# Kernel tuning notes

Hardware: AMD Instinct MI355X
Metric: run time of the kernel (lower is better)

Reference implementation:

```python
import jax, jax.numpy as jnp
import numpy as np
from jax import lax

B, T, N = 512, 512, 64  # batch, max_seq_len, num_tags


def setup_inputs() -> dict:
    key = jax.random.key(0)
    k1, k2, k3, k4 = jax.random.split(key, 4)
    inputs = jax.random.normal(k1, (B, T, N), dtype=jnp.float32)
    transition_params = jax.random.normal(k2, (N, N), dtype=jnp.float32)
    tag_indices = jax.random.randint(k3, (B, T), 0, N, dtype=jnp.int32)
    sequence_lengths = jax.random.randint(k4, (B,), 0, T, dtype=jnp.int32)
    return {
        "inputs": inputs,
        "transition_params": transition_params,
        "tag_indices": tag_indices,
        "sequence_lengths": sequence_lengths,
    }


def _crf_log_norm(inputs, transition_params, sequence_lengths):
    # inputs: [B, T, N]
    first = inputs[:, 0, :]                       # alpha after first token, [B, N]
    rest = jnp.transpose(inputs[:, 1:, :], (1, 0, 2))  # [T-1, B, N]

    def step(alpha, emit):
        # alpha: [B, N] -> broadcast-add transitions [N, N], logsumexp over prev tag
        new = emit + jax.nn.logsumexp(alpha[:, :, None] + transition_params[None], axis=1)
        return new, new

    _, alphas = lax.scan(step, first, rest)       # [T-1, B, N]
    all_alphas = jnp.concatenate([first[None], alphas], axis=0)  # [T, B, N]
    all_alphas = jnp.transpose(all_alphas, (1, 0, 2))            # [B, T, N]
    last_index = jnp.maximum(0, sequence_lengths - 1)            # [B]
    alpha_last = jnp.take_along_axis(all_alphas, last_index[:, None, None], axis=1)[:, 0, :]
    return jax.nn.logsumexp(alpha_last, axis=1)   # [B]


def _crf_sequence_score(inputs, tag_indices, sequence_lengths, transition_params):
    mask = (jnp.arange(T)[None, :] < sequence_lengths[:, None]).astype(inputs.dtype)  # [B, T]
    # unary: gather emission score of the gold tag at each position
    unary = jnp.take_along_axis(inputs, tag_indices[:, :, None], axis=2)[:, :, 0]      # [B, T]
    unary_scores = jnp.sum(unary * mask, axis=1)
    # binary: transition scores between consecutive gold tags
    binary = transition_params[tag_indices[:, :-1], tag_indices[:, 1:]]                # [B, T-1]
    binary_scores = jnp.sum(binary * mask[:, 1:], axis=1)
    return unary_scores + binary_scores


def reference(inputs, transition_params, tag_indices, sequence_lengths):
    tag_indices = tag_indices.astype(jnp.int32)
    sequence_lengths = sequence_lengths.astype(jnp.int32)
    sequence_scores = _crf_sequence_score(inputs, tag_indices, sequence_lengths, transition_params)
    log_norm = _crf_log_norm(inputs, transition_params, sequence_lengths)
    log_likelihood = sequence_scores - log_norm   # [B]
    return (log_likelihood, transition_params)
```

## Files before the change

### kernel.cpp

```cpp
#include <hip/hip_runtime.h>

#define BB 512
#define TT 512
#define NN 64

__device__ __forceinline__ float readlane_f(float v, int lane) {
    return __int_as_float(__builtin_amdgcn_readlane(__float_as_int(v), lane));
}


#define S2(x) #x
#define S1(x) S2(x)
#define RLX(SR, L) "v_readlane_b32 " SR ", %4, " S1(L) "\n\t"

#define SCLOB "s40","s41","s42","s43","s44","s45","s46","s47", \
              "s48","s49","s50","s51","s52","s53","s54","s55"

#define GRP0() \
    asm volatile( \
        "s_nop 4\n\t" \
        RLX("s40", 0)  RLX("s41", 1)  RLX("s42", 2)  RLX("s43", 3)  \
        RLX("s44", 4)  RLX("s45", 5)  RLX("s46", 6)  RLX("s47", 7)  \
        RLX("s48", 8)  RLX("s49", 9)  RLX("s50", 10) RLX("s51", 11) \
        RLX("s52", 12) RLX("s53", 13) RLX("s54", 14) RLX("s55", 15) \
        "v_pk_mul_f32 %0, s[40:41], %5\n\t" \
        "v_pk_mul_f32 %1, s[42:43], %6\n\t" \
        "v_pk_mul_f32 %2, s[44:45], %7\n\t" \
        "v_pk_mul_f32 %3, s[46:47], %8\n\t" \
        "v_pk_fma_f32 %0, s[48:49], %9,  %0\n\t" \
        "v_pk_fma_f32 %1, s[50:51], %10, %1\n\t" \
        "v_pk_fma_f32 %2, s[52:53], %11, %2\n\t" \
        "v_pk_fma_f32 %3, s[54:55], %12, %3\n\t" \
        : "=&v"(a0), "=&v"(a1), "=&v"(a2), "=&v"(a3) \
        : "v"(q), \
          "v"(EP[0]), "v"(EP[1]), "v"(EP[2]), "v"(EP[3]), \
          "v"(EP[4]), "v"(EP[5]), "v"(EP[6]), "v"(EP[7]) \
        : SCLOB);

#define GRPN(G) \
    asm volatile( \
        RLX("s40", (G)*16+0)  RLX("s41", (G)*16+1)  RLX("s42", (G)*16+2)  RLX("s43", (G)*16+3)  \
        RLX("s44", (G)*16+4)  RLX("s45", (G)*16+5)  RLX("s46", (G)*16+6)  RLX("s47", (G)*16+7)  \
        RLX("s48", (G)*16+8)  RLX("s49", (G)*16+9)  RLX("s50", (G)*16+10) RLX("s51", (G)*16+11) \
        RLX("s52", (G)*16+12) RLX("s53", (G)*16+13) RLX("s54", (G)*16+14) RLX("s55", (G)*16+15) \
        "v_pk_fma_f32 %0, s[40:41], %5,  %0\n\t" \
        "v_pk_fma_f32 %1, s[42:43], %6,  %1\n\t" \
        "v_pk_fma_f32 %2, s[44:45], %7,  %2\n\t" \
        "v_pk_fma_f32 %3, s[46:47], %8,  %3\n\t" \
        "v_pk_fma_f32 %0, s[48:49], %9,  %0\n\t" \
        "v_pk_fma_f32 %1, s[50:51], %10, %1\n\t" \
        "v_pk_fma_f32 %2, s[52:53], %11, %2\n\t" \
        "v_pk_fma_f32 %3, s[54:55], %12, %3\n\t" \
        : "+v"(a0), "+v"(a1), "+v"(a2), "+v"(a3) \
        : "v"(q), \
          "v"(EP[8*(G)+0]), "v"(EP[8*(G)+1]), "v"(EP[8*(G)+2]), "v"(EP[8*(G)+3]), \
          "v"(EP[8*(G)+4]), "v"(EP[8*(G)+5]), "v"(EP[8*(G)+6]), "v"(EP[8*(G)+7]) \
        : SCLOB);

#define STEP(tc_, EM) { \
    float2 a0, a1, a2, a3; \
    GRP0() GRPN(1) GRPN(2) GRPN(3) \
    const float sdot = ((a0.x + a0.y) + (a1.x + a1.y)) \
                     + ((a2.x + a2.y) + (a3.x + a3.y)); \
    const float s0v = readlane_f(sdot, 0); \
    const int   k   = ((__float_as_int(s0v) >> 23) & 255) - 127; \
    const bool  act = (tc_) <= last; \
    kcum += act ? k : 0; \
    const float qn = (EM) * ldexpf(sdot, -k); \
    q = act ? qn : q; \
}

__global__ __launch_bounds__(64, 1) void crf_kernel(
    const float* __restrict__ inputs,
    const float* __restrict__ trans,
    const int*   __restrict__ tags,
    const int*   __restrict__ lens,
    float*       __restrict__ out)
{
    const int b = blockIdx.x;
    const int j = threadIdx.x;

    if (b < 64) out[BB + b * 64 + j] = trans[b * 64 + j];

    const int L    = lens[b];
    const int last = (L - 1) > 0 ? (L - 1) : 0;

    const float* inb  = inputs + (size_t)b * TT * NN;
    const int*   tagb = tags + (size_t)b * TT;

    float sc = 0.f;
    #pragma unroll
    for (int k = 0; k < 8; ++k) {
        const int t  = k * 64 + j;
        const int tg = tagb[t];
        if (t < L) sc += inb[t * NN + tg];
        if (t + 1 < L) sc += trans[tg * NN + tagb[t + 1]];
    }
    #pragma unroll
    for (int x = 32; x >= 1; x >>= 1) sc += __shfl_xor(sc, x, 64);

    float2 EP[32];
    #pragma unroll
    for (int g = 0; g < 32; ++g) {
        EP[g].x = __expf(trans[(2 * g)     * NN + j]);
        EP[g].y = __expf(trans[(2 * g + 1) * NN + j]);
    }

    const float alpha0 = inb[j];
    const float m0 = readlane_f(alpha0, 0);
    float q = __expf(alpha0 - m0);
    int kcum = 0;

    float4 fA0, fA1, fB0, fB1;

#define LD(vec, comp, tt) { const int tc_ = (tt) <= last ? (tt) : last; \
                            vec.comp = inb[tc_ * NN + j]; }
#define LOAD8(v0, v1, base) \
    LD(v0, x, (base) + 0) LD(v0, y, (base) + 1) LD(v0, z, (base) + 2) LD(v0, w, (base) + 3) \
    LD(v1, x, (base) + 4) LD(v1, y, (base) + 5) LD(v1, z, (base) + 6) LD(v1, w, (base) + 7)
#define EXP8(v0, v1) \
    v0.x = __expf(v0.x); v0.y = __expf(v0.y); v0.z = __expf(v0.z); v0.w = __expf(v0.w); \
    v1.x = __expf(v1.x); v1.y = __expf(v1.y); v1.z = __expf(v1.z); v1.w = __expf(v1.w);

    LOAD8(fA0, fA1, 1)
    EXP8(fA0, fA1)

    for (int t0 = 1; t0 <= last; t0 += 16) {
        LOAD8(fB0, fB1, t0 + 8)
        STEP(t0 + 0, fA0.x) STEP(t0 + 1, fA0.y) STEP(t0 + 2, fA0.z) STEP(t0 + 3, fA0.w)
        STEP(t0 + 4, fA1.x) STEP(t0 + 5, fA1.y) STEP(t0 + 6, fA1.z) STEP(t0 + 7, fA1.w)
        EXP8(fB0, fB1)
        LOAD8(fA0, fA1, t0 + 16)
        STEP(t0 + 8,  fB0.x) STEP(t0 + 9,  fB0.y) STEP(t0 + 10, fB0.z) STEP(t0 + 11, fB0.w)
        STEP(t0 + 12, fB1.x) STEP(t0 + 13, fB1.y) STEP(t0 + 14, fB1.z) STEP(t0 + 15, fB1.w)
        EXP8(fA0, fA1)
    }
#undef EXP8
#undef LOAD8
#undef LD

    float qs = q;
    #pragma unroll
    for (int x = 32; x >= 1; x >>= 1) qs += __shfl_xor(qs, x, 64);
    if (j == 0) {
        const double C = (double)m0 + (double)kcum * 0.6931471805599453;
        out[b] = sc - (float)((double)__logf(qs) + C);
    }
}

extern "C" void kernel_launch(void* const* d_in, const int* in_sizes, int n_in,
                              void* d_out, int out_size, void* d_ws, size_t ws_size,
                              hipStream_t stream) {
    const float* inputs = (const float*)d_in[0];
    const float* trans  = (const float*)d_in[1];
    const int*   tags   = (const int*)d_in[2];
    const int*   lens   = (const int*)d_in[3];
    float*       out    = (float*)d_out;

    crf_kernel<<<dim3(BB), dim3(64), 0, stream>>>(inputs, trans, tags, lens, out);
}
```

Baseline: 237.6 us.

## Replace readlane broadcast matvec with DPP row-rotate FMAs and sparse rescaling

The per-timestep 64x64 exp-domain matvec no longer broadcasts q through 64 v_readlane instructions into scalar registers. Instead it uses three ds_bpermute calls to fetch q from the other 16-lane rows and v_fmac_f32_dpp with row_ror to rotate within each row. The exp-transition matrix is preloaded in a permuted layout matching the DPP rotation direction, which is detected at runtime. Power-of-two rescaling now runs every 4th step instead of every step, cutting readlane and exponent work but risking float overflow or underflow between rescales.

```diff
diff --git a/kernel.cpp b/kernel.cpp
--- a/kernel.cpp
+++ b/kernel.cpp
@@ -11,63 +11,57 @@
 
 #define S2(x) #x
 #define S1(x) S2(x)
-#define RLX(SR, L) "v_readlane_b32 " SR ", %4, " S1(L) "\n\t"
 
-#define SCLOB "s40","s41","s42","s43","s44","s45","s46","s47", \
-              "s48","s49","s50","s51","s52","s53","s54","s55"
+#define FMAC_DPP(ACC, QB, EV, R) \
+    asm("v_fmac_f32_dpp %0, %1, %2 row_ror:" S1(R) " row_mask:0xf bank_mask:0xf" \
+        : "+v"(ACC) : "v"(QB), "v"(EV));
+#define MUL_DPP(DST, QB, EV, R) \
+    asm("v_mul_f32_dpp %0, %1, %2 row_ror:" S1(R) " row_mask:0xf bank_mask:0xf" \
+        : "=v"(DST) : "v"(QB), "v"(EV));
 
-#define GRP0() \
-    asm volatile( \
-        "s_nop 4\n\t" \
-        RLX("s40", 0)  RLX("s41", 1)  RLX("s42", 2)  RLX("s43", 3)  \
-        RLX("s44", 4)  RLX("s45", 5)  RLX("s46", 6)  RLX("s47", 7)  \
-        RLX("s48", 8)  RLX("s49", 9)  RLX("s50", 10) RLX("s51", 11) \
-        RLX("s52", 12) RLX("s53", 13) RLX("s54", 14) RLX("s55", 15) \
-        "v_pk_mul_f32 %0, s[40:41], %5\n\t" \
-        "v_pk_mul_f32 %1, s[42:43], %6\n\t" \
-        "v_pk_mul_f32 %2, s[44:45], %7\n\t" \
-        "v_pk_mul_f32 %3, s[46:47], %8\n\t" \
-        "v_pk_fma_f32 %0, s[48:49], %9,  %0\n\t" \
-        "v_pk_fma_f32 %1, s[50:51], %10, %1\n\t" \
-        "v_pk_fma_f32 %2, s[52:53], %11, %2\n\t" \
-        "v_pk_fma_f32 %3, s[54:55], %12, %3\n\t" \
-        : "=&v"(a0), "=&v"(a1), "=&v"(a2), "=&v"(a3) \
-        : "v"(q), \
-          "v"(EP[0]), "v"(EP[1]), "v"(EP[2]), "v"(EP[3]), \
-          "v"(EP[4]), "v"(EP[5]), "v"(EP[6]), "v"(EP[7]) \
-        : SCLOB);
+#define BLK_FIRST(QB, C0, C1, C2, C3) \
+    a0 = QB * C0.x; \
+    MUL_DPP(a1, QB, C0.y, 1)  MUL_DPP(a2, QB, C0.z, 2)  MUL_DPP(a3, QB, C0.w, 3) \
+    FMAC_DPP(a0, QB, C1.x, 4)  FMAC_DPP(a1, QB, C1.y, 5) \
+    FMAC_DPP(a2, QB, C1.z, 6)  FMAC_DPP(a3, QB, C1.w, 7) \
+    FMAC_DPP(a0, QB, C2.x, 8)  FMAC_DPP(a1, QB, C2.y, 9) \
+    FMAC_DPP(a2, QB, C2.z, 10) FMAC_DPP(a3, QB, C2.w, 11) \
+    FMAC_DPP(a0, QB, C3.x, 12) FMAC_DPP(a1, QB, C3.y, 13) \
+    FMAC_DPP(a2, QB, C3.z, 14) FMAC_DPP(a3, QB, C3.w, 15)
 
-#define GRPN(G) \
-    asm volatile( \
-        RLX("s40", (G)*16+0)  RLX("s41", (G)*16+1)  RLX("s42", (G)*16+2)  RLX("s43", (G)*16+3)  \
-        RLX("s44", (G)*16+4)  RLX("s45", (G)*16+5)  RLX("s46", (G)*16+6)  RLX("s47", (G)*16+7)  \
-        RLX("s48", (G)*16+8)  RLX("s49", (G)*16+9)  RLX("s50", (G)*16+10) RLX("s51", (G)*16+11) \
-        RLX("s52", (G)*16+12) RLX("s53", (G)*16+13) RLX("s54", (G)*16+14) RLX("s55", (G)*16+15) \
-        "v_pk_fma_f32 %0, s[40:41], %5,  %0\n\t" \
-        "v_pk_fma_f32 %1, s[42:43], %6,  %1\n\t" \
-        "v_pk_fma_f32 %2, s[44:45], %7,  %2\n\t" \
-        "v_pk_fma_f32 %3, s[46:47], %8,  %3\n\t" \
-        "v_pk_fma_f32 %0, s[48:49], %9,  %0\n\t" \
-        "v_pk_fma_f32 %1, s[50:51], %10, %1\n\t" \
-        "v_pk_fma_f32 %2, s[52:53], %11, %2\n\t" \
-        "v_pk_fma_f32 %3, s[54:55], %12, %3\n\t" \
-        : "+v"(a0), "+v"(a1), "+v"(a2), "+v"(a3) \
-        : "v"(q), \
-          "v"(EP[8*(G)+0]), "v"(EP[8*(G)+1]), "v"(EP[8*(G)+2]), "v"(EP[8*(G)+3]), \
-          "v"(EP[8*(G)+4]), "v"(EP[8*(G)+5]), "v"(EP[8*(G)+6]), "v"(EP[8*(G)+7]) \
-        : SCLOB);
+#define BLK(QB, C0, C1, C2, C3) \
+    a0 = fmaf(QB, C0.x, a0); \
+    FMAC_DPP(a1, QB, C0.y, 1)  FMAC_DPP(a2, QB, C0.z, 2)  FMAC_DPP(a3, QB, C0.w, 3) \
+    FMAC_DPP(a0, QB, C1.x, 4)  FMAC_DPP(a1, QB, C1.y, 5) \
+    FMAC_DPP(a2, QB, C1.z, 6)  FMAC_DPP(a3, QB, C1.w, 7) \
+    FMAC_DPP(a0, QB, C2.x, 8)  FMAC_DPP(a1, QB, C2.y, 9) \
+    FMAC_DPP(a2, QB, C2.z, 10) FMAC_DPP(a3, QB, C2.w, 11) \
+    FMAC_DPP(a0, QB, C3.x, 12) FMAC_DPP(a1, QB, C3.y, 13) \
+    FMAC_DPP(a2, QB, C3.z, 14) FMAC_DPP(a3, QB, C3.w, 15)
 
-#define STEP(tc_, EM) { \
-    float2 a0, a1, a2, a3; \
-    GRP0() GRPN(1) GRPN(2) GRPN(3) \
-    const float sdot = ((a0.x + a0.y) + (a1.x + a1.y)) \
-                     + ((a2.x + a2.y) + (a3.x + a3.y)); \
-    const float s0v = readlane_f(sdot, 0); \
-    const int   k   = ((__float_as_int(s0v) >> 23) & 255) - 127; \
-    const bool  act = (tc_) <= last; \
-    kcum += act ? k : 0; \
-    const float qn = (EM) * ldexpf(sdot, -k); \
-    q = act ? qn : q; \
+#define STEP(tc_, EM, RESC) { \
+    asm("s_nop 1" : "+v"(q));    \
+    const int qi = __float_as_int(q); \
+    const float q1 = __int_as_float(__builtin_amdgcn_ds_bpermute(a16, qi)); \
+    const float q2 = __int_as_float(__builtin_amdgcn_ds_bpermute(a32, qi)); \
+    const float q3 = __int_as_float(__builtin_amdgcn_ds_bpermute(a48, qi)); \
+    float a0, a1, a2, a3; \
+    BLK_FIRST(q, D00, D01, D02, D03) \
+    BLK(q1, D10, D11, D12, D13) \
+    BLK(q2, D20, D21, D22, D23) \
+    BLK(q3, D30, D31, D32, D33) \
+    const float s = (a0 + a1) + (a2 + a3); \
+    float qn; \
+    if (RESC) { \
+        const int sb = __float_as_int(readlane_f(s, 0)); \
+        const int kb = ((sb >> 23) & 255) - 127; \
+        const float sf = __int_as_float((127 - kb) << 23);   \
+        qn = (s * (EM)) * sf; \
+        if ((tc_) <= last) kcum += kb; \
+    } else { \
+        qn = s * (EM); \
+    } \
+    q = ((tc_) <= last) ? qn : q; \
 }
 
 __global__ __launch_bounds__(64, 1) void crf_kernel(
@@ -99,12 +93,29 @@
     #pragma unroll
     for (int x = 32; x >= 1; x >>= 1) sc += __shfl_xor(sc, x, 64);
 
-    float2 EP[32];
-    #pragma unroll
-    for (int g = 0; g < 32; ++g) {
-        EP[g].x = __expf(trans[(2 * g)     * NN + j]);
-        EP[g].y = __expf(trans[(2 * g + 1) * NN + j]);
-    }
+    const int pr  = __builtin_amdgcn_update_dpp(0, j, 0x121 ,
+                                                0xf, 0xf, false);
+    const int r0p = __builtin_amdgcn_readlane(pr, 0);
+    const int dhw = (r0p == 1) ? 1 : -1;
+
+    float4 D00, D01, D02, D03, D10, D11, D12, D13;
+    float4 D20, D21, D22, D23, D30, D31, D32, D33;
+#define LDD(DST, B, R) { \
+    const int rr = (j + dhw * (R)) & 15; \
+    const int ii = (((j & 48) | rr) + 16 * (B)) & 63; \
+    DST = __expf(trans[ii * NN + j]); }
+#define LDD4(V, B, R0) LDD(V.x, B, R0) LDD(V.y, B, (R0)+1) \
+                       LDD(V.z, B, (R0)+2) LDD(V.w, B, (R0)+3)
+    LDD4(D00, 0, 0) LDD4(D01, 0, 4) LDD4(D02, 0, 8) LDD4(D03, 0, 12)
+    LDD4(D10, 1, 0) LDD4(D11, 1, 4) LDD4(D12, 1, 8) LDD4(D13, 1, 12)
+    LDD4(D20, 2, 0) LDD4(D21, 2, 4) LDD4(D22, 2, 8) LDD4(D23, 2, 12)
+    LDD4(D30, 3, 0) LDD4(D31, 3, 4) LDD4(D32, 3, 8) LDD4(D33, 3, 12)
+#undef LDD4
+#undef LDD
+
+    const int a16 = ((j + 16) & 63) * 4;
+    const int a32 = ((j + 32) & 63) * 4;
+    const int a48 = ((j + 48) & 63) * 4;
 
     const float alpha0 = inb[j];
     const float m0 = readlane_f(alpha0, 0);
@@ -127,12 +138,16 @@
 
     for (int t0 = 1; t0 <= last; t0 += 16) {
         LOAD8(fB0, fB1, t0 + 8)
-        STEP(t0 + 0, fA0.x) STEP(t0 + 1, fA0.y) STEP(t0 + 2, fA0.z) STEP(t0 + 3, fA0.w)
-        STEP(t0 + 4, fA1.x) STEP(t0 + 5, fA1.y) STEP(t0 + 6, fA1.z) STEP(t0 + 7, fA1.w)
+        STEP(t0 + 0, fA0.x, 0) STEP(t0 + 1, fA0.y, 0)
+        STEP(t0 + 2, fA0.z, 0) STEP(t0 + 3, fA0.w, 1)
+        STEP(t0 + 4, fA1.x, 0) STEP(t0 + 5, fA1.y, 0)
+        STEP(t0 + 6, fA1.z, 0) STEP(t0 + 7, fA1.w, 1)
         EXP8(fB0, fB1)
         LOAD8(fA0, fA1, t0 + 16)
-        STEP(t0 + 8,  fB0.x) STEP(t0 + 9,  fB0.y) STEP(t0 + 10, fB0.z) STEP(t0 + 11, fB0.w)
-        STEP(t0 + 12, fB1.x) STEP(t0 + 13, fB1.y) STEP(t0 + 14, fB1.z) STEP(t0 + 15, fB1.w)
+        STEP(t0 + 8,  fB0.x, 0) STEP(t0 + 9,  fB0.y, 0)
+        STEP(t0 + 10, fB0.z, 0) STEP(t0 + 11, fB0.w, 1)
+        STEP(t0 + 12, fB1.x, 0) STEP(t0 + 13, fB1.y, 0)
+        STEP(t0 + 14, fB1.z, 0) STEP(t0 + 15, fB1.w, 1)
         EXP8(fA0, fA1)
     }
 #undef EXP8
```

Result: faster. 202.7 us (-14.7%).
